# Kernel tuning notes

Hardware: AMD Instinct MI355X
Metric: run time of the kernel (lower is better)

## Reference

```python
import jax, jax.numpy as jnp
import numpy as np

# SOM hyperparameters (match init_kwargs)
M, N = 64, 64
NODES = M * N
FEATS = 256
BATCH = 1024
LR = 0.5
RADIUS_FACTOR = 1.1
TOTAL_ITER = 100000
SIGMA = max(M, N) * RADIUS_FACTOR


def setup_inputs() -> dict:
    key = jax.random.key(0)
    k1, k2 = jax.random.split(key)
    x = jax.random.uniform(k1, (BATCH, FEATS), dtype=jnp.float32)
    map_w = jax.random.uniform(k2, (NODES, FEATS), dtype=jnp.float32)
    return {"x": x, "map_w": map_w, "iteration": 0}


def _grid_locs():
    ii, jj = jnp.meshgrid(jnp.arange(M), jnp.arange(N), indexing='ij')
    return jnp.stack([ii.ravel(), jj.ravel()], axis=1)  # (NODES, 2) int32


def reference(x, map_w, iteration):
    B = x.shape[0]
    # ---- feedforward: squared distances (B, NODES) via GEMM expansion,
    # avoiding the (B, NODES, FEATS) broadcast the TF code materializes.
    x2 = jnp.sum(x * x, axis=1, keepdims=True)          # (B, 1)
    w2 = jnp.sum(map_w * map_w, axis=1)                  # (NODES,)
    sqd = x2 + w2[None, :] - 2.0 * (x @ map_w.T)         # (B, NODES)
    bmu_indices = jnp.argmin(sqd, axis=1)                # (B,)

    # ---- backprop: neighborhood-weighted codebook update
    locs = _grid_locs()                                  # (NODES, 2)
    bmu_locs = locs[bmu_indices]                         # (B, 2)
    # grid distance^2 between every node and each sample's BMU: (B, NODES)
    d2 = jnp.sum((locs[None, :, :] - bmu_locs[:, None, :]) ** 2, axis=2).astype(jnp.float32)

    lambda_g = TOTAL_ITER / SIGMA
    decay = jnp.exp(jnp.float32(-float(iteration) / lambda_g))
    radius = SIGMA * decay + 1e-6
    lr = LR * decay

    impact = jnp.exp(-d2 / (2.0 * radius * radius))
    in_radius = (jnp.sqrt(d2) <= radius).astype(jnp.float32)
    lr_op = impact * in_radius * lr                      # (B, NODES)

    # weight_update[n,d] = sum_b lr_op[b,n] * (x[b,d] - map_w[n,d])
    # computed without the (B, NODES, FEATS) intermediate:
    upd = (jnp.einsum('bn,bd->nd', lr_op, x) - lr_op.sum(axis=0)[:, None] * map_w) / B
    new_map = map_w + upd
    return new_map, bmu_indices
```

## Files before the change

### kernel.cpp

```cpp
#include <hip/hip_runtime.h>
#include <math.h>

#define NODES 4096
#define FEATS 256
#define BATCH 1024
#define LR_C 0.5f
#define SIGMA_C 70.4f

typedef _Float16 f16x8 __attribute__((ext_vector_type(8)));
typedef float floatx4 __attribute__((ext_vector_type(4)));

__device__ __forceinline__ void get_params(int it, float& lr, float& r2, float& i2r2) {
    float decay = __expf(-(float)it * (SIGMA_C / 100000.0f));
    float radius = SIGMA_C * decay + 1e-6f;
    lr = LR_C * decay;
    r2 = radius * radius;
    i2r2 = 1.0f / (2.0f * r2);
}

__device__ __forceinline__ unsigned fkey(float f) {
    unsigned u = __float_as_uint(f);
    return (u & 0x80000000u) ? ~u : (u | 0x80000000u);
}
__device__ __forceinline__ unsigned long long shfl_xor_u64(unsigned long long v, int mask) {
    unsigned lo = (unsigned)v, hi = (unsigned)(v >> 32);
    lo = __shfl_xor(lo, mask, 64);
    hi = __shfl_xor(hi, mask, 64);
    return ((unsigned long long)hi << 32) | lo;
}

__global__ __launch_bounds__(256) void k_prep(const float* __restrict__ Wm, const float* __restrict__ X,
                                              _Float16* __restrict__ Whi, _Float16* __restrict__ Wlo,
                                              float* __restrict__ w2,
                                              _Float16* __restrict__ Xhi, _Float16* __restrict__ Xlo,
                                              _Float16* __restrict__ XT,
                                              unsigned long long* __restrict__ gmin) {
    __shared__ _Float16 T[64][72];
    const int t = threadIdx.x;
    const int blk = blockIdx.x;
    const int wave = t >> 6, lane = t & 63;
#pragma unroll
    for (int rr = 0; rr < 2; ++rr) {
        int row = blk * 8 + wave * 2 + rr;
        float4 v = *(const float4*)&Wm[(size_t)row * FEATS + lane * 4];
        union { _Float16 h[4]; float2 f2; } uh, ul;
        uh.h[0] = (_Float16)v.x; uh.h[1] = (_Float16)v.y;
        uh.h[2] = (_Float16)v.z; uh.h[3] = (_Float16)v.w;
        ul.h[0] = (_Float16)(v.x - (float)uh.h[0]);
        ul.h[1] = (_Float16)(v.y - (float)uh.h[1]);
        ul.h[2] = (_Float16)(v.z - (float)uh.h[2]);
        ul.h[3] = (_Float16)(v.w - (float)uh.h[3]);
        *(float2*)&Whi[(size_t)row * FEATS + lane * 4] = uh.f2;
        *(float2*)&Wlo[(size_t)row * FEATS + lane * 4] = ul.f2;
        float s = v.x * v.x + v.y * v.y + v.z * v.z + v.w * v.w;
#pragma unroll
        for (int off = 32; off > 0; off >>= 1) s += __shfl_down(s, off, 64);
        if (lane == 0) w2[row] = s;
    }
    if (blk < 4) gmin[blk * 256 + t] = 0xFFFFFFFFFFFFFFFFULL;
    if (blk < 64) {
        const int b0 = (blk & 15) * 64, d0 = (blk >> 4) * 64;
        {
            const int bl = t >> 2, dq = (t & 3) * 16;
            union { _Float16 h[16]; float4 q[2]; } uh, ul;
#pragma unroll
            for (int c = 0; c < 4; ++c) {
                float4 v = *(const float4*)&X[(size_t)(b0 + bl) * FEATS + d0 + dq + c * 4];
                uh.h[c * 4 + 0] = (_Float16)v.x; uh.h[c * 4 + 1] = (_Float16)v.y;
                uh.h[c * 4 + 2] = (_Float16)v.z; uh.h[c * 4 + 3] = (_Float16)v.w;
                ul.h[c * 4 + 0] = (_Float16)(v.x - (float)uh.h[c * 4 + 0]);
                ul.h[c * 4 + 1] = (_Float16)(v.y - (float)uh.h[c * 4 + 1]);
                ul.h[c * 4 + 2] = (_Float16)(v.z - (float)uh.h[c * 4 + 2]);
                ul.h[c * 4 + 3] = (_Float16)(v.w - (float)uh.h[c * 4 + 3]);
            }
            *(float4*)&Xhi[(size_t)(b0 + bl) * FEATS + d0 + dq] = uh.q[0];
            *(float4*)&Xhi[(size_t)(b0 + bl) * FEATS + d0 + dq + 8] = uh.q[1];
            *(float4*)&Xlo[(size_t)(b0 + bl) * FEATS + d0 + dq] = ul.q[0];
            *(float4*)&Xlo[(size_t)(b0 + bl) * FEATS + d0 + dq + 8] = ul.q[1];
#pragma unroll
            for (int c = 0; c < 16; ++c) T[bl][dq + c] = uh.h[c];
        }
        __syncthreads();
        {
            const int dl = t >> 2, bq = (t & 3) * 16;
            union { _Float16 h[16]; float4 q[2]; } u;
#pragma unroll
            for (int c = 0; c < 16; ++c) u.h[c] = T[bq + c][dl];
            *(float4*)&XT[(size_t)(d0 + dl) * BATCH + b0 + bq] = u.q[0];
            *(float4*)&XT[(size_t)(d0 + dl) * BATCH + b0 + bq + 8] = u.q[1];
        }
    }
}

__global__ __launch_bounds__(256) void k_gemm1min(const _Float16* __restrict__ Xhi, const _Float16* __restrict__ Xlo,
                                                  const _Float16* __restrict__ Whi, const _Float16* __restrict__ Wlo,
                                                  const float* __restrict__ w2,
                                                  unsigned long long* __restrict__ gmin) {
    __shared__ _Float16 Ah[64][40];
    __shared__ _Float16 Al[64][40];
    __shared__ _Float16 Bh[64][40];
    __shared__ _Float16 Bl[64][40];
    __shared__ unsigned long long rowmin[64][2];
    const int n0 = blockIdx.x * 64;
    const int b0 = blockIdx.y * 64;
    const int t = threadIdx.x;
    const int wave = t >> 6, lane = t & 63;
    const int wm = wave & 1, wn = wave >> 1;
    const int lm = lane & 15, quad = lane >> 4;
    const int srow = t >> 2, skoff = (t & 3) * 8;
    floatx4 acc[2][2] = {};
    for (int k0 = 0; k0 < FEATS; k0 += 32) {
        *(float4*)&Ah[srow][skoff] = *(const float4*)&Xhi[(size_t)(b0 + srow) * FEATS + k0 + skoff];
        *(float4*)&Al[srow][skoff] = *(const float4*)&Xlo[(size_t)(b0 + srow) * FEATS + k0 + skoff];
        *(float4*)&Bh[srow][skoff] = *(const float4*)&Whi[(size_t)(n0 + srow) * FEATS + k0 + skoff];
        *(float4*)&Bl[srow][skoff] = *(const float4*)&Wlo[(size_t)(n0 + srow) * FEATS + k0 + skoff];
        __syncthreads();
        f16x8 ah[2], al[2], bh[2], bl[2];
        ah[0] = *(f16x8*)&Ah[wm * 32 + lm][quad * 8];
        ah[1] = *(f16x8*)&Ah[wm * 32 + 16 + lm][quad * 8];
        al[0] = *(f16x8*)&Al[wm * 32 + lm][quad * 8];
        al[1] = *(f16x8*)&Al[wm * 32 + 16 + lm][quad * 8];
        bh[0] = *(f16x8*)&Bh[wn * 32 + lm][quad * 8];
        bh[1] = *(f16x8*)&Bh[wn * 32 + 16 + lm][quad * 8];
        bl[0] = *(f16x8*)&Bl[wn * 32 + lm][quad * 8];
        bl[1] = *(f16x8*)&Bl[wn * 32 + 16 + lm][quad * 8];
#pragma unroll
        for (int i = 0; i < 2; ++i)
#pragma unroll
            for (int j = 0; j < 2; ++j) {
                acc[i][j] = __builtin_amdgcn_mfma_f32_16x16x32_f16(ah[i], bh[j], acc[i][j], 0, 0, 0);
                acc[i][j] = __builtin_amdgcn_mfma_f32_16x16x32_f16(ah[i], bl[j], acc[i][j], 0, 0, 0);
                acc[i][j] = __builtin_amdgcn_mfma_f32_16x16x32_f16(al[i], bh[j], acc[i][j], 0, 0, 0);
            }
        __syncthreads();
    }
    const int col0 = n0 + wn * 32 + lm, col1 = col0 + 16;
    const float w20 = w2[col0], w21 = w2[col1];
#pragma unroll
    for (int i = 0; i < 2; ++i) {
#pragma unroll
        for (int r = 0; r < 4; ++r) {
            float va = w20 - 2.0f * acc[i][0][r];
            float vb = w21 - 2.0f * acc[i][1][r];
            unsigned long long ka = ((unsigned long long)fkey(va) << 32) | (unsigned)col0;
            unsigned long long kb = ((unsigned long long)fkey(vb) << 32) | (unsigned)col1;
            unsigned long long m = ka < kb ? ka : kb;
#pragma unroll
            for (int mk = 1; mk < 16; mk <<= 1) {
                unsigned long long o = shfl_xor_u64(m, mk);
                if (o < m) m = o;
            }
            if (lm == 0) rowmin[wm * 32 + i * 16 + quad * 4 + r][wn] = m;
        }
    }
    __syncthreads();
    if (t < 64) {
        unsigned long long v = rowmin[t][0];
        if (rowmin[t][1] < v) v = rowmin[t][1];
        atomicMin(&gmin[b0 + t], v);
    }
}

__global__ __launch_bounds__(256) void k_lropB(const unsigned long long* __restrict__ gmin,
                                               const int* __restrict__ itp,
                                               _Float16* __restrict__ lrT, float* __restrict__ Svec,
                                               float* __restrict__ out1) {
    __shared__ int bmu_s[1024];
    __shared__ float texp[64];
    __shared__ float red4[4];
    const int t = threadIdx.x;
    const int blk = blockIdx.x;
#pragma unroll
    for (int j = 0; j < 4; ++j)
        bmu_s[t + j * 256] = (int)(gmin[t + j * 256] & 0xFFFFFFFFULL);
    float lr, r2, i2r2;
    get_params(itp[0], lr, r2, i2r2);
    if (t < 64) texp[t] = __expf(-(float)(t * t) * i2r2);
    __syncthreads();
    if (blk < 4) out1[blk * 256 + t] = (float)bmu_s[blk * 256 + t];
    const int n = blk * 2 + (t >> 7);
    const int b0 = (t & 127) * 8;
    const int ni = n >> 6, nj = n & 63;
    float s = 0.0f;
    union { _Float16 h[8]; float4 q; } u;
#pragma unroll
    for (int c = 0; c < 8; ++c) {
        int m = bmu_s[b0 + c];
        int di = ni - (m >> 6); di = di < 0 ? -di : di;
        int dj = nj - (m & 63); dj = dj < 0 ? -dj : dj;
        int d2 = di * di + dj * dj;
        float val = ((float)d2 <= r2) ? lr * texp[di] * texp[dj] : 0.0f;
        u.h[c] = (_Float16)val;
        s += val;
    }
    *(float4*)&lrT[(size_t)n * BATCH + b0] = u.q;
    const int lane = t & 63, wave = t >> 6;
#pragma unroll
    for (int off = 32; off > 0; off >>= 1) s += __shfl_down(s, off, 64);
    if (lane == 0) red4[wave] = s;
    __syncthreads();
    if (t < 2) Svec[blk * 2 + t] = red4[2 * t] + red4[2 * t + 1];
}

__global__ __launch_bounds__(256) void k_gemm2c(const _Float16* __restrict__ lrT, const _Float16* __restrict__ XT,
                                                const float* __restrict__ Svec, const float* __restrict__ Wm,
                                                float* __restrict__ out0) {
    __shared__ _Float16 As[32][136];
    __shared__ _Float16 Bs[64][136];
    __shared__ float Svl[32];
    const int d0 = blockIdx.x * 64;
    const int n0 = blockIdx.y * 32;
    const int t = threadIdx.x;
    const int wave = t >> 6, lane = t & 63;
    const int wm = wave & 1, wn = wave >> 1;
    const int lm = lane & 15, quad = lane >> 4;
    if (t < 32) Svl[t] = Svec[n0 + t];
    const int arow = t >> 3, acoff = (t & 7) * 16;
    const int brow = t >> 2, bcoff = (t & 3) * 32;
    floatx4 acc0 = {}, acc1 = {};
    for (int k0 = 0; k0 < BATCH; k0 += 128) {
        *(float4*)&As[arow][acoff] = *(const float4*)&lrT[(size_t)(n0 + arow) * BATCH + k0 + acoff];
        *(float4*)&As[arow][acoff + 8] = *(const float4*)&lrT[(size_t)(n0 + arow) * BATCH + k0 + acoff + 8];
#pragma unroll
        for (int c = 0; c < 4; ++c)
            *(float4*)&Bs[brow][bcoff + c * 8] =
                *(const float4*)&XT[(size_t)(d0 + brow) * BATCH + k0 + bcoff + c * 8];
        __syncthreads();
#pragma unroll
        for (int ks = 0; ks < 128; ks += 32) {
            f16x8 a = *(f16x8*)&As[wm * 16 + lm][ks + quad * 8];
            f16x8 b0 = *(f16x8*)&Bs[wn * 32 + lm][ks + quad * 8];
            f16x8 b1 = *(f16x8*)&Bs[wn * 32 + 16 + lm][ks + quad * 8];
            acc0 = __builtin_amdgcn_mfma_f32_16x16x32_f16(a, b0, acc0, 0, 0, 0);
            acc1 = __builtin_amdgcn_mfma_f32_16x16x32_f16(a, b1, acc1, 0, 0, 0);
        }
        __syncthreads();
    }
    const float invB = 1.0f / (float)BATCH;
#pragma unroll
    for (int r = 0; r < 4; ++r) {
        int rowN = n0 + wm * 16 + quad * 4 + r;
        float cc = 1.0f - Svl[rowN - n0] * invB;
        int col0 = d0 + wn * 32 + lm;
        int col1 = col0 + 16;
        out0[(size_t)rowN * FEATS + col0] = Wm[(size_t)rowN * FEATS + col0] * cc + acc0[r] * invB;
        out0[(size_t)rowN * FEATS + col1] = Wm[(size_t)rowN * FEATS + col1] * cc + acc1[r] * invB;
    }
}

extern "C" void kernel_launch(void* const* d_in, const int* in_sizes, int n_in,
                              void* d_out, int out_size, void* d_ws, size_t ws_size,
                              hipStream_t stream) {
    const float* X = (const float*)d_in[0];
    const float* Wm = (const float*)d_in[1];
    const int* itp = (const int*)d_in[2];
    float* out0 = (float*)d_out;
    float* out1 = out0 + (size_t)NODES * FEATS;

    char* ws = (char*)d_ws;
    float* w2       = (float*)(ws + 0);
    _Float16* Xhi   = (_Float16*)(ws + 16384);
    _Float16* Xlo   = (_Float16*)(ws + 540672);
    _Float16* XT    = (_Float16*)(ws + 1064960);
    _Float16* Whi   = (_Float16*)(ws + 1589248);
    _Float16* Wlo   = (_Float16*)(ws + 3686400);
    unsigned long long* gmin = (unsigned long long*)(ws + 5783552);
    float* Svec     = (float*)(ws + 5791744);
    _Float16* lrT   = (_Float16*)(ws + 5808128);

    k_prep<<<512, 256, 0, stream>>>(Wm, X, Whi, Wlo, w2, Xhi, Xlo, XT, gmin);
    k_gemm1min<<<dim3(64, 16), 256, 0, stream>>>(Xhi, Xlo, Whi, Wlo, w2, gmin);
    k_lropB<<<2048, 256, 0, stream>>>(gmin, itp, lrT, Svec, out1);
    k_gemm2c<<<dim3(4, 128), 256, 0, stream>>>(lrT, XT, Svec, Wm, out0);
}
```

Before: 95.74 us.

## Fuse neighborhood-weight computation into second GEMM, removing lrT intermediate

Drops the separate kernel that built the fp16 neighborhood-weight matrix and its row sums. The GEMM2 kernel now computes those weights on the fly from the BMU indices while filling its A tile in shared memory. Row sums are built with a shuffle reduction. This removes one launch and the write and read of an 8 MB intermediate. In exchange, each of the 4 column blocks recomputes the same weights and calls exp per element instead of using a lookup table.

```diff
diff --git a/kernel.cpp b/kernel.cpp
--- a/kernel.cpp
+++ b/kernel.cpp
@@ -161,52 +161,14 @@
     }
 }
 
-__global__ __launch_bounds__(256) void k_lropB(const unsigned long long* __restrict__ gmin,
-                                               const int* __restrict__ itp,
-                                               _Float16* __restrict__ lrT, float* __restrict__ Svec,
-                                               float* __restrict__ out1) {
-    __shared__ int bmu_s[1024];
-    __shared__ float texp[64];
-    __shared__ float red4[4];
-    const int t = threadIdx.x;
-    const int blk = blockIdx.x;
-#pragma unroll
-    for (int j = 0; j < 4; ++j)
-        bmu_s[t + j * 256] = (int)(gmin[t + j * 256] & 0xFFFFFFFFULL);
-    float lr, r2, i2r2;
-    get_params(itp[0], lr, r2, i2r2);
-    if (t < 64) texp[t] = __expf(-(float)(t * t) * i2r2);
-    __syncthreads();
-    if (blk < 4) out1[blk * 256 + t] = (float)bmu_s[blk * 256 + t];
-    const int n = blk * 2 + (t >> 7);
-    const int b0 = (t & 127) * 8;
-    const int ni = n >> 6, nj = n & 63;
-    float s = 0.0f;
-    union { _Float16 h[8]; float4 q; } u;
-#pragma unroll
-    for (int c = 0; c < 8; ++c) {
-        int m = bmu_s[b0 + c];
-        int di = ni - (m >> 6); di = di < 0 ? -di : di;
-        int dj = nj - (m & 63); dj = dj < 0 ? -dj : dj;
-        int d2 = di * di + dj * dj;
-        float val = ((float)d2 <= r2) ? lr * texp[di] * texp[dj] : 0.0f;
-        u.h[c] = (_Float16)val;
-        s += val;
-    }
-    *(float4*)&lrT[(size_t)n * BATCH + b0] = u.q;
-    const int lane = t & 63, wave = t >> 6;
-#pragma unroll
-    for (int off = 32; off > 0; off >>= 1) s += __shfl_down(s, off, 64);
-    if (lane == 0) red4[wave] = s;
-    __syncthreads();
-    if (t < 2) Svec[blk * 2 + t] = red4[2 * t] + red4[2 * t + 1];
-}
-
-__global__ __launch_bounds__(256) void k_gemm2c(const _Float16* __restrict__ lrT, const _Float16* __restrict__ XT,
-                                                const float* __restrict__ Svec, const float* __restrict__ Wm,
-                                                float* __restrict__ out0) {
+__global__ __launch_bounds__(256) void k_gemm2f(const _Float16* __restrict__ XT,
+                                                const unsigned long long* __restrict__ gmin,
+                                                const int* __restrict__ itp,
+                                                const float* __restrict__ Wm,
+                                                float* __restrict__ out0, float* __restrict__ out1) {
     __shared__ _Float16 As[32][136];
     __shared__ _Float16 Bs[64][136];
+    __shared__ int bmu_s[1024];
     __shared__ float Svl[32];
     const int d0 = blockIdx.x * 64;
     const int n0 = blockIdx.y * 32;
@@ -214,13 +176,37 @@
     const int wave = t >> 6, lane = t & 63;
     const int wm = wave & 1, wn = wave >> 1;
     const int lm = lane & 15, quad = lane >> 4;
-    if (t < 32) Svl[t] = Svec[n0 + t];
-    const int arow = t >> 3, acoff = (t & 7) * 16;
+
+#pragma unroll
+    for (int j = 0; j < 4; ++j)
+        bmu_s[t + j * 256] = (int)(gmin[t + j * 256] & 0xFFFFFFFFULL);
+    float lr, r2, i2r2;
+    get_params(itp[0], lr, r2, i2r2);
+    if (blockIdx.x == 0 && blockIdx.y < 4)
+        out1[blockIdx.y * 256 + t] = (float)(int)(gmin[blockIdx.y * 256 + t] & 0xFFFFFFFFULL);
+    __syncthreads();
+
+    const int arow = t >> 3, ac = (t & 7) * 16;
+    const int nn = n0 + arow;
+    const int ni = nn >> 6, nj = nn & 63;
     const int brow = t >> 2, bcoff = (t & 3) * 32;
+
+    float ssum = 0.0f;
     floatx4 acc0 = {}, acc1 = {};
     for (int k0 = 0; k0 < BATCH; k0 += 128) {
-        *(float4*)&As[arow][acoff] = *(const float4*)&lrT[(size_t)(n0 + arow) * BATCH + k0 + acoff];
-        *(float4*)&As[arow][acoff + 8] = *(const float4*)&lrT[(size_t)(n0 + arow) * BATCH + k0 + acoff + 8];
+        union { _Float16 h[16]; float4 q[2]; } u;
+#pragma unroll
+        for (int c = 0; c < 16; ++c) {
+            int m = bmu_s[k0 + ac + c];
+            int di = ni - (m >> 6); di = di < 0 ? -di : di;
+            int dj = nj - (m & 63); dj = dj < 0 ? -dj : dj;
+            float d2f = (float)(di * di + dj * dj);
+            float val = (d2f <= r2) ? lr * __expf(-d2f * i2r2) : 0.0f;
+            u.h[c] = (_Float16)val;
+            ssum += val;
+        }
+        *(float4*)&As[arow][ac] = u.q[0];
+        *(float4*)&As[arow][ac + 8] = u.q[1];
 #pragma unroll
         for (int c = 0; c < 4; ++c)
             *(float4*)&Bs[brow][bcoff + c * 8] =
@@ -236,6 +222,11 @@
         }
         __syncthreads();
     }
+#pragma unroll
+    for (int mk = 1; mk < 8; mk <<= 1) ssum += __shfl_xor(ssum, mk, 64);
+    if ((t & 7) == 0) Svl[arow] = ssum;
+    __syncthreads();
+
     const float invB = 1.0f / (float)BATCH;
 #pragma unroll
     for (int r = 0; r < 4; ++r) {
@@ -265,11 +256,8 @@
     _Float16* Whi   = (_Float16*)(ws + 1589248);
     _Float16* Wlo   = (_Float16*)(ws + 3686400);
     unsigned long long* gmin = (unsigned long long*)(ws + 5783552);
-    float* Svec     = (float*)(ws + 5791744);
-    _Float16* lrT   = (_Float16*)(ws + 5808128);
 
     k_prep<<<512, 256, 0, stream>>>(Wm, X, Whi, Wlo, w2, Xhi, Xlo, XT, gmin);
     k_gemm1min<<<dim3(64, 16), 256, 0, stream>>>(Xhi, Xlo, Whi, Wlo, w2, gmin);
-    k_lropB<<<2048, 256, 0, stream>>>(gmin, itp, lrT, Svec, out1);
-    k_gemm2c<<<dim3(4, 128), 256, 0, stream>>>(lrT, XT, Svec, Wm, out0);
-}
+    k_gemm2f<<<dim3(4, 128), 256, 0, stream>>>(XT, gmin, itp, Wm, out0, out1);
+}
```

Result: faster. 92.05 us (-3.9%).
